# Optimization experiments

Hardware: AMD Instinct MI355X
Metric: run time of the kernel (lower is better)

Reference implementation:

```python
import jax, jax.numpy as jnp
import numpy as np

D_MODEL = 1024
N_HEAD = 16
HEAD_DIM = D_MODEL // N_HEAD


def setup_inputs() -> dict:
    key = jax.random.key(0)
    ks = jax.random.split(key, 11)
    B, L = 1, 2048
    s = 1.0 / np.sqrt(D_MODEL)
    return {
        "q": jax.random.normal(ks[0], (B, L, D_MODEL), jnp.float32),
        "k": jax.random.normal(ks[1], (B, L, D_MODEL), jnp.float32),
        "v": jax.random.normal(ks[2], (B, L, D_MODEL), jnp.float32),
        "w_q": jax.random.normal(ks[3], (D_MODEL, D_MODEL), jnp.float32) * s,
        "b_q": jax.random.normal(ks[4], (D_MODEL,), jnp.float32) * s,
        "w_k": jax.random.normal(ks[5], (D_MODEL, D_MODEL), jnp.float32) * s,
        "b_k": jax.random.normal(ks[6], (D_MODEL,), jnp.float32) * s,
        "w_v": jax.random.normal(ks[7], (D_MODEL, D_MODEL), jnp.float32) * s,
        "b_v": jax.random.normal(ks[8], (D_MODEL,), jnp.float32) * s,
        "w_o": jax.random.normal(ks[9], (D_MODEL, D_MODEL), jnp.float32) * s,
        "b_o": jax.random.normal(ks[10], (D_MODEL,), jnp.float32) * s,
    }


def _split_heads(x):
    # [B, L, D] -> [B, H, L, Dh]
    B, L, D = x.shape
    return x.reshape(B, L, N_HEAD, HEAD_DIM).transpose(0, 2, 1, 3)


def reference(q, k, v, w_q, b_q, w_k, b_k, w_v, b_v, w_o, b_o):
    # Linear projections (torch Linear: x @ W.T + b; here weights stored as [D_in, D_out])
    qh = _split_heads(q @ w_q + b_q)
    kh = _split_heads(k @ w_k + b_k)
    vh = _split_heads(v @ w_v + b_v)
    scale = 1.0 / jnp.sqrt(jnp.asarray(HEAD_DIM, qh.dtype))
    # [B, H, Lq, Lk] full score matrix (faithful to naive implementation)
    score = jnp.einsum("bhqd,bhkd->bhqk", qh, kh) * scale
    attn = jax.nn.softmax(score, axis=-1)
    out = jnp.einsum("bhqk,bhkd->bhqd", attn, vh)
    # concat heads: [B, H, L, Dh] -> [B, L, D]
    B, H, L, Dh = out.shape
    out = out.transpose(0, 2, 1, 3).reshape(B, L, H * Dh)
    return out @ w_o + b_o  # dropout p=0.0 -> identity
```

## Files before the change

### kernel.cpp

```cpp
#include <hip/hip_runtime.h>
#include <hip/hip_bf16.h>
#include <stdint.h>
#include <stddef.h>

typedef __bf16 bf16_t;
typedef __bf16 v8bf __attribute__((ext_vector_type(8)));
typedef __bf16 v4bf __attribute__((ext_vector_type(4)));
typedef float  v4f  __attribute__((ext_vector_type(4)));

#define L_SEQ 2048
#define DM    1024
#define NH    16
#define LOG2E 1.44269504088896340736f
#define SCL   (0.125f * LOG2E)

__device__ __forceinline__ void async_cp16(const void* g, void* l) {
  __builtin_amdgcn_global_load_lds(
      (__attribute__((address_space(1))) void*)(g),
      (__attribute__((address_space(3))) void*)(l),
      16, 0, 0);
}

__device__ __forceinline__ v4f mfma16(v8bf a, v8bf b, v4f c) {
  return __builtin_amdgcn_mfma_f32_16x16x32_bf16(a, b, c, 0, 0, 0);
}

__global__ void k_prep(
    const float* __restrict__ q, const float* __restrict__ k,
    const float* __restrict__ v,
    const float* __restrict__ w0, const float* __restrict__ w1,
    const float* __restrict__ w2, const float* __restrict__ w3,
    bf16_t* __restrict__ Qb, bf16_t* __restrict__ Kb, bf16_t* __restrict__ Vb,
    bf16_t* __restrict__ o0, bf16_t* __restrict__ o1,
    bf16_t* __restrict__ o2, bf16_t* __restrict__ o3)
{
  const int z = blockIdx.z;
  const int tid = threadIdx.x;
  if (z < 4) {
    const float* in = (z == 0) ? w0 : (z == 1) ? w1 : (z == 2) ? w2 : w3;
    bf16_t*     out = (z == 0) ? o0 : (z == 1) ? o1 : (z == 2) ? o2 : o3;
    __shared__ float t[64 * 65];
    const int r0 = blockIdx.y * 64, c0 = blockIdx.x * 64;
#pragma unroll
    for (int p = 0; p < 16; ++p) {
      const int idx = p * 256 + tid;
      const int r = idx >> 6, c = idx & 63;
      t[r * 65 + c] = in[(size_t)(r0 + r) * DM + c0 + c];
    }
    __syncthreads();
#pragma unroll
    for (int p = 0; p < 16; ++p) {
      const int idx = p * 256 + tid;
      const int c = idx >> 6, r = idx & 63;
      out[(size_t)(c0 + c) * DM + r0 + r] = (bf16_t)t[r * 65 + c];
    }
  } else {
    const float* src = (z == 4) ? q : (z == 5) ? k : v;
    bf16_t*      dst = (z == 4) ? Qb : (z == 5) ? Kb : Vb;
    const int n4 = (L_SEQ * DM) / 4;
    const int base = (blockIdx.y * 16 + blockIdx.x) * 256 + tid;
#pragma unroll
    for (int i = base; i < n4; i += 16 * 16 * 256) {
      v4f x = ((const v4f*)src)[i];
      v4bf y;
      y[0] = (bf16_t)x[0]; y[1] = (bf16_t)x[1];
      y[2] = (bf16_t)x[2]; y[3] = (bf16_t)x[3];
      ((v4bf*)dst)[i] = y;
    }
  }
}

__global__ void k_transpose(const bf16_t* __restrict__ in, bf16_t* __restrict__ out,
                            int R, int Cc)
{
  __shared__ bf16_t t[64 * 66];
  const int tid = threadIdx.x;
  const int r0 = blockIdx.y * 64, c0 = blockIdx.x * 64;
#pragma unroll
  for (int p = 0; p < 16; ++p) {
    const int idx = p * 256 + tid;
    const int r = idx >> 6, c = idx & 63;
    t[r * 66 + c] = in[(size_t)(r0 + r) * Cc + c0 + c];
  }
  __syncthreads();
#pragma unroll
  for (int p = 0; p < 16; ++p) {
    const int idx = p * 256 + tid;
    const int c = idx >> 6, r = idx & 63;
    out[(size_t)(c0 + c) * R + r0 + r] = t[r * 66 + c];
  }
}

template <typename OutT>
__device__ __forceinline__ void gemm_body(
    const bf16_t* __restrict__ A, const bf16_t* __restrict__ Bt,
    const float* __restrict__ bias, OutT* __restrict__ C,
    int M, int N, int K, int bx, int by)
{
  __shared__ __align__(16) bf16_t As[2][128 * 64];
  __shared__ __align__(16) bf16_t Bs[2][64 * 64];
  const int tid  = threadIdx.x;
  const int w    = tid >> 6;
  const int lane = tid & 63;
  const int l16  = lane & 15;
  const int q4   = lane >> 4;
  const int m0   = by * 128, n0 = bx * 64;
  const int wm   = (w >> 1) * 64, wn = (w & 1) * 32;

  v4f acc[4][2];
#pragma unroll
  for (int i = 0; i < 4; ++i)
#pragma unroll
    for (int j = 0; j < 2; ++j) {
      v4f z = {0.f, 0.f, 0.f, 0.f};
      acc[i][j] = z;
    }

  const int lr = lane >> 3;
  const int lc = lane & 7;

  auto stage = [&](int k0, int buf) {
#pragma unroll
    for (int c = 0; c < 4; ++c) {
      const int row = 32 * w + 8 * c + lr;
      const int q   = lc ^ (row & 7);
      async_cp16(A + (size_t)(m0 + row) * K + k0 + q * 8,
                 &As[buf][(32 * w + 8 * c) * 64]);
    }
#pragma unroll
    for (int c = 0; c < 2; ++c) {
      const int row = 16 * w + 8 * c + lr;
      const int q   = lc ^ (row & 7);
      async_cp16(Bt + (size_t)(n0 + row) * K + k0 + q * 8,
                 &Bs[buf][(16 * w + 8 * c) * 64]);
    }
  };

  stage(0, 0);
  __syncthreads();

  const int nk = K >> 6;
  for (int kt = 0; kt < nk; ++kt) {
    if (kt + 1 < nk) stage((kt + 1) << 6, (kt + 1) & 1);
    const int buf = kt & 1;
#pragma unroll
    for (int ks = 0; ks < 2; ++ks) {
      v8bf af[4], bf_[2];
#pragma unroll
      for (int mi = 0; mi < 4; ++mi) {
        const int row = wm + mi * 16 + l16;
        const int pc  = (4 * ks + q4) ^ (row & 7);
        af[mi] = *(const v8bf*)(&As[buf][row * 64 + pc * 8]);
      }
#pragma unroll
      for (int ni = 0; ni < 2; ++ni) {
        const int row = wn + ni * 16 + l16;
        const int pc  = (4 * ks + q4) ^ (row & 7);
        bf_[ni] = *(const v8bf*)(&Bs[buf][row * 64 + pc * 8]);
      }
#pragma unroll
      for (int mi = 0; mi < 4; ++mi)
#pragma unroll
        for (int ni = 0; ni < 2; ++ni)
          acc[mi][ni] = mfma16(af[mi], bf_[ni], acc[mi][ni]);
    }
    __syncthreads();
  }

  float bv[2];
#pragma unroll
  for (int ni = 0; ni < 2; ++ni) bv[ni] = bias[n0 + wn + ni * 16 + l16];
#pragma unroll
  for (int mi = 0; mi < 4; ++mi) {
#pragma unroll
    for (int r = 0; r < 4; ++r) {
      const int row = m0 + wm + mi * 16 + q4 * 4 + r;
#pragma unroll
      for (int ni = 0; ni < 2; ++ni) {
        const int col = n0 + wn + ni * 16 + l16;
        C[(size_t)row * N + col] = (OutT)(acc[mi][ni][r] + bv[ni]);
      }
    }
  }
}

__global__ __launch_bounds__(256, 3) void k_gemm_f32out(
    const bf16_t* __restrict__ A, const bf16_t* __restrict__ Bt,
    const float* __restrict__ bias, float* __restrict__ C,
    int M, int N, int K)
{
  gemm_body<float>(A, Bt, bias, C, M, N, K, blockIdx.x, blockIdx.y);
}

__global__ __launch_bounds__(256, 3) void k_gemm_qkv(
    const bf16_t* __restrict__ q, const bf16_t* __restrict__ k,
    const bf16_t* __restrict__ v,
    const bf16_t* __restrict__ wqt, const bf16_t* __restrict__ wkt,
    const bf16_t* __restrict__ wvt,
    const float* __restrict__ bq, const float* __restrict__ bk,
    const float* __restrict__ bv,
    bf16_t* __restrict__ Qp, bf16_t* __restrict__ Kp, bf16_t* __restrict__ Vp)
{
  const int z = blockIdx.z;
  const bf16_t* A    = (z == 0) ? q   : (z == 1) ? k   : v;
  const bf16_t* Bt   = (z == 0) ? wqt : (z == 1) ? wkt : wvt;
  const float*  bias = (z == 0) ? bq  : (z == 1) ? bk  : bv;
  bf16_t*       C    = (z == 0) ? Qp  : (z == 1) ? Kp  : Vp;
  gemm_body<bf16_t>(A, Bt, bias, C, L_SEQ, DM, DM, blockIdx.x, blockIdx.y);
}

__global__ __launch_bounds__(256, 2) void k_attn(
    const bf16_t* __restrict__ Qp,
    const bf16_t* __restrict__ Kp,
    const bf16_t* __restrict__ Vt,
    bf16_t* __restrict__ AO)
{
  const int h  = blockIdx.y;
  const int q0 = blockIdx.x * 64;
  const int tid = threadIdx.x, w = tid >> 6, lane = tid & 63;
  const int l16 = lane & 15, q4 = lane >> 4;
  const int lr = lane >> 3, lc = lane & 7;

  __shared__ __align__(16) bf16_t Qs[64 * 64];
  __shared__ __align__(16) bf16_t Ks[2][64 * 64];
  __shared__ __align__(16) bf16_t Vs[2][64 * 64];
  __shared__ __align__(16) bf16_t Ps[64 * 72];

  auto stage_kv = [&](int j0, int buf) {
#pragma unroll
    for (int c = 0; c < 2; ++c) {
      const int row = 16 * w + 8 * c + lr;
      const int q   = lc ^ (row & 7);
      async_cp16(Kp + (size_t)(j0 + row) * DM + h * 64 + q * 8,
                 &Ks[buf][(16 * w + 8 * c) * 64]);
      async_cp16(Vt + (size_t)(h * 64 + row) * L_SEQ + j0 + q * 8,
                 &Vs[buf][(16 * w + 8 * c) * 64]);
    }
  };

#pragma unroll
  for (int c = 0; c < 2; ++c) {
    const int row = 16 * w + 8 * c + lr;
    const int q   = lc ^ (row & 7);
    async_cp16(Qp + (size_t)(q0 + row) * DM + h * 64 + q * 8,
               &Qs[(16 * w + 8 * c) * 64]);
  }
  stage_kv(0, 0);
  __syncthreads();

  v8bf bq[2];
  {
    const int rowq = 16 * w + l16;
#pragma unroll
    for (int ks = 0; ks < 2; ++ks) {
      const int pc = (4 * ks + q4) ^ (rowq & 7);
      bq[ks] = *(const v8bf*)(&Qs[rowq * 64 + pc * 8]);
    }
  }

  float m_run = -1e30f, l_run = 0.f;
  v4f od[4];
#pragma unroll
  for (int d = 0; d < 4; ++d) { v4f z = {0.f,0.f,0.f,0.f}; od[d] = z; }

  const int prow = 16 * w + l16;

  for (int jt = 0; jt < L_SEQ / 64; ++jt) {
    if (jt + 1 < L_SEQ / 64) stage_kv((jt + 1) * 64, (jt + 1) & 1);
    const int buf = jt & 1;

    v4f st[4];
#pragma unroll
    for (int nf = 0; nf < 4; ++nf) {
      v4f a0 = {0.f, 0.f, 0.f, 0.f};
#pragma unroll
      for (int ks = 0; ks < 2; ++ks) {
        const int rowk = nf * 16 + l16;
        const int pc   = (4 * ks + q4) ^ (rowk & 7);
        v8bf ak = *(const v8bf*)(&Ks[buf][rowk * 64 + pc * 8]);
        a0 = mfma16(ak, bq[ks], a0);
      }
      st[nf] = a0;
    }

    float mx = st[0][0];
#pragma unroll
    for (int nf = 0; nf < 4; ++nf)
#pragma unroll
      for (int r = 0; r < 4; ++r) mx = fmaxf(mx, st[nf][r]);
    mx = fmaxf(mx, __shfl_xor(mx, 16, 64));
    mx = fmaxf(mx, __shfl_xor(mx, 32, 64));
    const float mn    = fmaxf(m_run, mx);
    const float alpha = exp2f((m_run - mn) * SCL);
    const float mnS   = mn * SCL;
    m_run = mn;

    float ps = 0.f;
#pragma unroll
    for (int nf = 0; nf < 4; ++nf) {
      v4bf pb;
#pragma unroll
      for (int r = 0; r < 4; ++r) {
        const float p = exp2f(fmaf(st[nf][r], SCL, -mnS));
        ps += p;
        pb[r] = (bf16_t)p;
      }
      *(v4bf*)(&Ps[prow * 72 + nf * 16 + q4 * 4]) = pb;
    }
    l_run = l_run * alpha + ps;
#pragma unroll
    for (int d = 0; d < 4; ++d)
#pragma unroll
      for (int r = 0; r < 4; ++r) od[d][r] *= alpha;

#pragma unroll
    for (int ks = 0; ks < 2; ++ks) {
      v8bf bp = *(const v8bf*)(&Ps[prow * 72 + ks * 32 + q4 * 8]);
#pragma unroll
      for (int dd = 0; dd < 4; ++dd) {
        const int rowv = dd * 16 + l16;
        const int pc   = (4 * ks + q4) ^ (rowv & 7);
        v8bf av = *(const v8bf*)(&Vs[buf][rowv * 64 + pc * 8]);
        od[dd] = mfma16(av, bp, od[dd]);
      }
    }
    __syncthreads();
  }

  l_run += __shfl_xor(l_run, 16, 64);
  l_run += __shfl_xor(l_run, 32, 64);
  const float inv = 1.f / l_run;

  const int rowo = q0 + 16 * w + l16;
#pragma unroll
  for (int dd = 0; dd < 4; ++dd) {
    v4bf ob;
#pragma unroll
    for (int r = 0; r < 4; ++r) ob[r] = (bf16_t)(od[dd][r] * inv);
    *(v4bf*)(&AO[(size_t)rowo * DM + h * 64 + dd * 16 + q4 * 4]) = ob;
  }
}

extern "C" void kernel_launch(void* const* d_in, const int* in_sizes, int n_in,
                              void* d_out, int out_size, void* d_ws, size_t ws_size,
                              hipStream_t stream)
{
  const float* q  = (const float*)d_in[0];
  const float* k  = (const float*)d_in[1];
  const float* v  = (const float*)d_in[2];
  const float* wq = (const float*)d_in[3];
  const float* bq = (const float*)d_in[4];
  const float* wk = (const float*)d_in[5];
  const float* bk = (const float*)d_in[6];
  const float* wv = (const float*)d_in[7];
  const float* bv = (const float*)d_in[8];
  const float* wo = (const float*)d_in[9];
  const float* bo = (const float*)d_in[10];
  float* out = (float*)d_out;

  bf16_t* ws  = (bf16_t*)d_ws;
  bf16_t* Qb  = ws;
  bf16_t* Kb  = Qb  + (size_t)L_SEQ * DM;
  bf16_t* Vb  = Kb  + (size_t)L_SEQ * DM;
  bf16_t* Qp  = Vb  + (size_t)L_SEQ * DM;
  bf16_t* Kp  = Qp  + (size_t)L_SEQ * DM;
  bf16_t* Vp  = Kp  + (size_t)L_SEQ * DM;
  bf16_t* Vtr = Vp  + (size_t)L_SEQ * DM;
  bf16_t* AO  = Vtr + (size_t)L_SEQ * DM;
  bf16_t* Wqt = AO  + (size_t)L_SEQ * DM;
  bf16_t* Wkt = Wqt + (size_t)DM * DM;
  bf16_t* Wvt = Wkt + (size_t)DM * DM;
  bf16_t* Wot = Wvt + (size_t)DM * DM;

  k_prep<<<dim3(16, 16, 7), 256, 0, stream>>>(q, k, v, wq, wk, wv, wo,
                                              Qb, Kb, Vb, Wqt, Wkt, Wvt, Wot);
  k_gemm_qkv<<<dim3(16, 16, 3), 256, 0, stream>>>(Qb, Kb, Vb, Wqt, Wkt, Wvt,
                                                  bq, bk, bv, Qp, Kp, Vp);
  k_transpose<<<dim3(16, 32), 256, 0, stream>>>(Vp, Vtr, L_SEQ, DM);
  k_attn<<<dim3(32, 16), 256, 0, stream>>>(Qp, Kp, Vtr, AO);
  k_gemm_f32out<<<dim3(16, 16), 256, 0, stream>>>(AO, Wot, bo, out,
                                                  L_SEQ, DM, DM);
}
```

Measured before the change: 188.0 us.

## Retile GEMMs to 128-wide N with K=32 stages and halve attention block warps

The GEMM body becomes templated on the per-warp M extent. It uses 128-column N tiles and 32-deep K stages with a new swizzle and precomputed global pointers, so each warp holds a larger accumulator tile and reuses fragments more. The QKV GEMM uses 128x128 tiles and the output GEMM 64x128, with the grids adjusted to match. The attention kernel now runs 2 warps per block, each handling 32 query rows as two 16-row groups, so every K/V fragment read from LDS feeds two MFMAs. In exchange there is more register pressure, fewer blocks in flight, and twice as many K-loop barriers in the GEMMs.

```diff
diff --git a/kernel.cpp b/kernel.cpp
--- a/kernel.cpp
+++ b/kernel.cpp
@@ -91,92 +91,98 @@
   }
 }
 
-template <typename OutT>
+template <int MW, typename OutT>
 __device__ __forceinline__ void gemm_body(
     const bf16_t* __restrict__ A, const bf16_t* __restrict__ Bt,
     const float* __restrict__ bias, OutT* __restrict__ C,
     int M, int N, int K, int bx, int by)
 {
-  __shared__ __align__(16) bf16_t As[2][128 * 64];
-  __shared__ __align__(16) bf16_t Bs[2][64 * 64];
+  constexpr int MT = 2 * MW;
+  constexpr int CA = MW / 32;
+  constexpr int MI = MW / 16;
+  __shared__ __align__(16) bf16_t As[2][MT * 32];
+  __shared__ __align__(16) bf16_t Bs[2][128 * 32];
   const int tid  = threadIdx.x;
   const int w    = tid >> 6;
   const int lane = tid & 63;
   const int l16  = lane & 15;
   const int q4   = lane >> 4;
-  const int m0   = by * 128, n0 = bx * 64;
-  const int wm   = (w >> 1) * 64, wn = (w & 1) * 32;
-
-  v4f acc[4][2];
-#pragma unroll
-  for (int i = 0; i < 4; ++i)
-#pragma unroll
-    for (int j = 0; j < 2; ++j) {
+  const int m0   = by * MT, n0 = bx * 128;
+  const int wm   = (w >> 1) * MW, wn = (w & 1) * 64;
+
+  v4f acc[MI][4];
+#pragma unroll
+  for (int i = 0; i < MI; ++i)
+#pragma unroll
+    for (int j = 0; j < 4; ++j) {
       v4f z = {0.f, 0.f, 0.f, 0.f};
       acc[i][j] = z;
     }
 
-  const int lr = lane >> 3;
-  const int lc = lane & 7;
+  const int srow = lane >> 2;
+  const int sq   = lane & 3;
+  const bf16_t* pA[CA];
+  const bf16_t* pB[2];
+#pragma unroll
+  for (int c = 0; c < CA; ++c) {
+    const int row = (MW / 2) * w + 16 * c + srow;
+    const int q   = sq ^ ((row >> 1) & 3);
+    pA[c] = A + (size_t)(m0 + row) * K + q * 8;
+  }
+#pragma unroll
+  for (int c = 0; c < 2; ++c) {
+    const int row = 32 * w + 16 * c + srow;
+    const int q   = sq ^ ((row >> 1) & 3);
+    pB[c] = Bt + (size_t)(n0 + row) * K + q * 8;
+  }
 
   auto stage = [&](int k0, int buf) {
 #pragma unroll
-    for (int c = 0; c < 4; ++c) {
-      const int row = 32 * w + 8 * c + lr;
-      const int q   = lc ^ (row & 7);
-      async_cp16(A + (size_t)(m0 + row) * K + k0 + q * 8,
-                 &As[buf][(32 * w + 8 * c) * 64]);
-    }
-#pragma unroll
-    for (int c = 0; c < 2; ++c) {
-      const int row = 16 * w + 8 * c + lr;
-      const int q   = lc ^ (row & 7);
-      async_cp16(Bt + (size_t)(n0 + row) * K + k0 + q * 8,
-                 &Bs[buf][(16 * w + 8 * c) * 64]);
-    }
+    for (int c = 0; c < CA; ++c)
+      async_cp16(pA[c] + k0, &As[buf][((MW / 2) * w + 16 * c) * 32]);
+#pragma unroll
+    for (int c = 0; c < 2; ++c)
+      async_cp16(pB[c] + k0, &Bs[buf][(32 * w + 16 * c) * 32]);
   };
 
   stage(0, 0);
   __syncthreads();
 
-  const int nk = K >> 6;
+  const int nk = K >> 5;
   for (int kt = 0; kt < nk; ++kt) {
-    if (kt + 1 < nk) stage((kt + 1) << 6, (kt + 1) & 1);
+    if (kt + 1 < nk) stage((kt + 1) << 5, (kt + 1) & 1);
     const int buf = kt & 1;
-#pragma unroll
-    for (int ks = 0; ks < 2; ++ks) {
-      v8bf af[4], bf_[2];
-#pragma unroll
-      for (int mi = 0; mi < 4; ++mi) {
-        const int row = wm + mi * 16 + l16;
-        const int pc  = (4 * ks + q4) ^ (row & 7);
-        af[mi] = *(const v8bf*)(&As[buf][row * 64 + pc * 8]);
-      }
-#pragma unroll
-      for (int ni = 0; ni < 2; ++ni) {
-        const int row = wn + ni * 16 + l16;
-        const int pc  = (4 * ks + q4) ^ (row & 7);
-        bf_[ni] = *(const v8bf*)(&Bs[buf][row * 64 + pc * 8]);
-      }
-#pragma unroll
-      for (int mi = 0; mi < 4; ++mi)
-#pragma unroll
-        for (int ni = 0; ni < 2; ++ni)
-          acc[mi][ni] = mfma16(af[mi], bf_[ni], acc[mi][ni]);
-    }
+    v8bf af[MI], bfr[4];
+#pragma unroll
+    for (int mi = 0; mi < MI; ++mi) {
+      const int row = wm + mi * 16 + l16;
+      const int qq  = q4 ^ ((row >> 1) & 3);
+      af[mi] = *(const v8bf*)(&As[buf][row * 32 + qq * 8]);
+    }
+#pragma unroll
+    for (int ni = 0; ni < 4; ++ni) {
+      const int row = wn + ni * 16 + l16;
+      const int qq  = q4 ^ ((row >> 1) & 3);
+      bfr[ni] = *(const v8bf*)(&Bs[buf][row * 32 + qq * 8]);
+    }
+#pragma unroll
+    for (int mi = 0; mi < MI; ++mi)
+#pragma unroll
+      for (int ni = 0; ni < 4; ++ni)
+        acc[mi][ni] = mfma16(af[mi], bfr[ni], acc[mi][ni]);
     __syncthreads();
   }
 
-  float bv[2];
-#pragma unroll
-  for (int ni = 0; ni < 2; ++ni) bv[ni] = bias[n0 + wn + ni * 16 + l16];
-#pragma unroll
-  for (int mi = 0; mi < 4; ++mi) {
+  float bv[4];
+#pragma unroll
+  for (int ni = 0; ni < 4; ++ni) bv[ni] = bias[n0 + wn + ni * 16 + l16];
+#pragma unroll
+  for (int mi = 0; mi < MI; ++mi) {
 #pragma unroll
     for (int r = 0; r < 4; ++r) {
       const int row = m0 + wm + mi * 16 + q4 * 4 + r;
 #pragma unroll
-      for (int ni = 0; ni < 2; ++ni) {
+      for (int ni = 0; ni < 4; ++ni) {
         const int col = n0 + wn + ni * 16 + l16;
         C[(size_t)row * N + col] = (OutT)(acc[mi][ni][r] + bv[ni]);
       }
@@ -184,15 +190,15 @@
   }
 }
 
-__global__ __launch_bounds__(256, 3) void k_gemm_f32out(
+__global__ __launch_bounds__(256, 2) void k_gemm_f32out(
     const bf16_t* __restrict__ A, const bf16_t* __restrict__ Bt,
     const float* __restrict__ bias, float* __restrict__ C,
     int M, int N, int K)
 {
-  gemm_body<float>(A, Bt, bias, C, M, N, K, blockIdx.x, blockIdx.y);
-}
-
-__global__ __launch_bounds__(256, 3) void k_gemm_qkv(
+  gemm_body<32, float>(A, Bt, bias, C, M, N, K, blockIdx.x, blockIdx.y);
+}
+
+__global__ __launch_bounds__(256, 2) void k_gemm_qkv(
     const bf16_t* __restrict__ q, const bf16_t* __restrict__ k,
     const bf16_t* __restrict__ v,
     const bf16_t* __restrict__ wqt, const bf16_t* __restrict__ wkt,
@@ -206,10 +212,10 @@
   const bf16_t* Bt   = (z == 0) ? wqt : (z == 1) ? wkt : wvt;
   const float*  bias = (z == 0) ? bq  : (z == 1) ? bk  : bv;
   bf16_t*       C    = (z == 0) ? Qp  : (z == 1) ? Kp  : Vp;
-  gemm_body<bf16_t>(A, Bt, bias, C, L_SEQ, DM, DM, blockIdx.x, blockIdx.y);
-}
-
-__global__ __launch_bounds__(256, 2) void k_attn(
+  gemm_body<64, bf16_t>(A, Bt, bias, C, L_SEQ, DM, DM, blockIdx.x, blockIdx.y);
+}
+
+__global__ __launch_bounds__(128, 2) void k_attn(
     const bf16_t* __restrict__ Qp,
     const bf16_t* __restrict__ Kp,
     const bf16_t* __restrict__ Vt,
@@ -226,118 +232,138 @@
   __shared__ __align__(16) bf16_t Vs[2][64 * 64];
   __shared__ __align__(16) bf16_t Ps[64 * 72];
 
+  const bf16_t* pK[4];
+  const bf16_t* pV[4];
+#pragma unroll
+  for (int c = 0; c < 4; ++c) {
+    const int row = 32 * w + 8 * c + lr;
+    const int q   = lc ^ (row & 7);
+    pK[c] = Kp + (size_t)row * DM + h * 64 + q * 8;
+    pV[c] = Vt + (size_t)(h * 64 + row) * L_SEQ + q * 8;
+  }
   auto stage_kv = [&](int j0, int buf) {
 #pragma unroll
-    for (int c = 0; c < 2; ++c) {
-      const int row = 16 * w + 8 * c + lr;
-      const int q   = lc ^ (row & 7);
-      async_cp16(Kp + (size_t)(j0 + row) * DM + h * 64 + q * 8,
-                 &Ks[buf][(16 * w + 8 * c) * 64]);
-      async_cp16(Vt + (size_t)(h * 64 + row) * L_SEQ + j0 + q * 8,
-                 &Vs[buf][(16 * w + 8 * c) * 64]);
+    for (int c = 0; c < 4; ++c) {
+      async_cp16(pK[c] + (size_t)j0 * DM, &Ks[buf][(32 * w + 8 * c) * 64]);
+      async_cp16(pV[c] + j0,              &Vs[buf][(32 * w + 8 * c) * 64]);
     }
   };
 
 #pragma unroll
-  for (int c = 0; c < 2; ++c) {
-    const int row = 16 * w + 8 * c + lr;
+  for (int c = 0; c < 4; ++c) {
+    const int row = 32 * w + 8 * c + lr;
     const int q   = lc ^ (row & 7);
     async_cp16(Qp + (size_t)(q0 + row) * DM + h * 64 + q * 8,
-               &Qs[(16 * w + 8 * c) * 64]);
+               &Qs[(32 * w + 8 * c) * 64]);
   }
   stage_kv(0, 0);
   __syncthreads();
 
-  v8bf bq[2];
-  {
-    const int rowq = 16 * w + l16;
+  v8bf bq[2][2];
+  const int prow0 = 32 * w + l16;
+  const int prow1 = 32 * w + 16 + l16;
+#pragma unroll
+  for (int g = 0; g < 2; ++g) {
+    const int rowq = 32 * w + 16 * g + l16;
 #pragma unroll
     for (int ks = 0; ks < 2; ++ks) {
       const int pc = (4 * ks + q4) ^ (rowq & 7);
-      bq[ks] = *(const v8bf*)(&Qs[rowq * 64 + pc * 8]);
-    }
-  }
-
-  float m_run = -1e30f, l_run = 0.f;
-  v4f od[4];
-#pragma unroll
-  for (int d = 0; d < 4; ++d) { v4f z = {0.f,0.f,0.f,0.f}; od[d] = z; }
-
-  const int prow = 16 * w + l16;
+      bq[g][ks] = *(const v8bf*)(&Qs[rowq * 64 + pc * 8]);
+    }
+  }
+
+  float m_run[2] = {-1e30f, -1e30f}, l_run[2] = {0.f, 0.f};
+  v4f od[2][4];
+#pragma unroll
+  for (int g = 0; g < 2; ++g)
+#pragma unroll
+    for (int d = 0; d < 4; ++d) { v4f z = {0.f,0.f,0.f,0.f}; od[g][d] = z; }
 
   for (int jt = 0; jt < L_SEQ / 64; ++jt) {
     if (jt + 1 < L_SEQ / 64) stage_kv((jt + 1) * 64, (jt + 1) & 1);
     const int buf = jt & 1;
 
-    v4f st[4];
+    v4f st[2][4];
+#pragma unroll
+    for (int g = 0; g < 2; ++g)
+#pragma unroll
+      for (int nf = 0; nf < 4; ++nf) { v4f z = {0.f,0.f,0.f,0.f}; st[g][nf] = z; }
 #pragma unroll
     for (int nf = 0; nf < 4; ++nf) {
-      v4f a0 = {0.f, 0.f, 0.f, 0.f};
+      const int rowk = nf * 16 + l16;
 #pragma unroll
       for (int ks = 0; ks < 2; ++ks) {
-        const int rowk = nf * 16 + l16;
-        const int pc   = (4 * ks + q4) ^ (rowk & 7);
+        const int pc = (4 * ks + q4) ^ (rowk & 7);
         v8bf ak = *(const v8bf*)(&Ks[buf][rowk * 64 + pc * 8]);
-        a0 = mfma16(ak, bq[ks], a0);
+        st[0][nf] = mfma16(ak, bq[0][ks], st[0][nf]);
+        st[1][nf] = mfma16(ak, bq[1][ks], st[1][nf]);
       }
-      st[nf] = a0;
-    }
-
-    float mx = st[0][0];
-#pragma unroll
-    for (int nf = 0; nf < 4; ++nf)
-#pragma unroll
-      for (int r = 0; r < 4; ++r) mx = fmaxf(mx, st[nf][r]);
-    mx = fmaxf(mx, __shfl_xor(mx, 16, 64));
-    mx = fmaxf(mx, __shfl_xor(mx, 32, 64));
-    const float mn    = fmaxf(m_run, mx);
-    const float alpha = exp2f((m_run - mn) * SCL);
-    const float mnS   = mn * SCL;
-    m_run = mn;
-
-    float ps = 0.f;
-#pragma unroll
-    for (int nf = 0; nf < 4; ++nf) {
-      v4bf pb;
-#pragma unroll
-      for (int r = 0; r < 4; ++r) {
-        const float p = exp2f(fmaf(st[nf][r], SCL, -mnS));
-        ps += p;
-        pb[r] = (bf16_t)p;
+    }
+
+#pragma unroll
+    for (int g = 0; g < 2; ++g) {
+      float mx = st[g][0][0];
+#pragma unroll
+      for (int nf = 0; nf < 4; ++nf)
+#pragma unroll
+        for (int r = 0; r < 4; ++r) mx = fmaxf(mx, st[g][nf][r]);
+      mx = fmaxf(mx, __shfl_xor(mx, 16, 64));
+      mx = fmaxf(mx, __shfl_xor(mx, 32, 64));
+      const float mn    = fmaxf(m_run[g], mx);
+      const float alpha = exp2f((m_run[g] - mn) * SCL);
+      const float mnS   = mn * SCL;
+      m_run[g] = mn;
+
+      const int prow = (g == 0) ? prow0 : prow1;
+      float ps = 0.f;
+#pragma unroll
+      for (int nf = 0; nf < 4; ++nf) {
+        v4bf pb;
+#pragma unroll
+        for (int r = 0; r < 4; ++r) {
+          const float p = exp2f(fmaf(st[g][nf][r], SCL, -mnS));
+          ps += p;
+          pb[r] = (bf16_t)p;
+        }
+        *(v4bf*)(&Ps[prow * 72 + nf * 16 + q4 * 4]) = pb;
       }
-      *(v4bf*)(&Ps[prow * 72 + nf * 16 + q4 * 4]) = pb;
-    }
-    l_run = l_run * alpha + ps;
-#pragma unroll
-    for (int d = 0; d < 4; ++d)
-#pragma unroll
-      for (int r = 0; r < 4; ++r) od[d][r] *= alpha;
+      l_run[g] = l_run[g] * alpha + ps;
+#pragma unroll
+      for (int d = 0; d < 4; ++d)
+#pragma unroll
+        for (int r = 0; r < 4; ++r) od[g][d][r] *= alpha;
+    }
 
 #pragma unroll
     for (int ks = 0; ks < 2; ++ks) {
-      v8bf bp = *(const v8bf*)(&Ps[prow * 72 + ks * 32 + q4 * 8]);
+      v8bf bp0 = *(const v8bf*)(&Ps[prow0 * 72 + ks * 32 + q4 * 8]);
+      v8bf bp1 = *(const v8bf*)(&Ps[prow1 * 72 + ks * 32 + q4 * 8]);
 #pragma unroll
       for (int dd = 0; dd < 4; ++dd) {
         const int rowv = dd * 16 + l16;
         const int pc   = (4 * ks + q4) ^ (rowv & 7);
         v8bf av = *(const v8bf*)(&Vs[buf][rowv * 64 + pc * 8]);
-        od[dd] = mfma16(av, bp, od[dd]);
+        od[0][dd] = mfma16(av, bp0, od[0][dd]);
+        od[1][dd] = mfma16(av, bp1, od[1][dd]);
       }
     }
     __syncthreads();
   }
 
-  l_run += __shfl_xor(l_run, 16, 64);
-  l_run += __shfl_xor(l_run, 32, 64);
-  const float inv = 1.f / l_run;
-
-  const int rowo = q0 + 16 * w + l16;
-#pragma unroll
-  for (int dd = 0; dd < 4; ++dd) {
-    v4bf ob;
-#pragma unroll
-    for (int r = 0; r < 4; ++r) ob[r] = (bf16_t)(od[dd][r] * inv);
-    *(v4bf*)(&AO[(size_t)rowo * DM + h * 64 + dd * 16 + q4 * 4]) = ob;
+#pragma unroll
+  for (int g = 0; g < 2; ++g) {
+    float l = l_run[g];
+    l += __shfl_xor(l, 16, 64);
+    l += __shfl_xor(l, 32, 64);
+    const float inv = 1.f / l;
+    const int rowo = q0 + 32 * w + 16 * g + l16;
+#pragma unroll
+    for (int dd = 0; dd < 4; ++dd) {
+      v4bf ob;
+#pragma unroll
+      for (int r = 0; r < 4; ++r) ob[r] = (bf16_t)(od[g][dd][r] * inv);
+      *(v4bf*)(&AO[(size_t)rowo * DM + h * 64 + dd * 16 + q4 * 4]) = ob;
+    }
   }
 }
 
@@ -374,10 +400,10 @@
 
   k_prep<<<dim3(16, 16, 7), 256, 0, stream>>>(q, k, v, wq, wk, wv, wo,
                                               Qb, Kb, Vb, Wqt, Wkt, Wvt, Wot);
-  k_gemm_qkv<<<dim3(16, 16, 3), 256, 0, stream>>>(Qb, Kb, Vb, Wqt, Wkt, Wvt,
-                                                  bq, bk, bv, Qp, Kp, Vp);
+  k_gemm_qkv<<<dim3(8, 16, 3), 256, 0, stream>>>(Qb, Kb, Vb, Wqt, Wkt, Wvt,
+                                                 bq, bk, bv, Qp, Kp, Vp);
   k_transpose<<<dim3(16, 32), 256, 0, stream>>>(Vp, Vtr, L_SEQ, DM);
-  k_attn<<<dim3(32, 16), 256, 0, stream>>>(Qp, Kp, Vtr, AO);
-  k_gemm_f32out<<<dim3(16, 16), 256, 0, stream>>>(AO, Wot, bo, out,
-                                                  L_SEQ, DM, DM);
-}
+  k_attn<<<dim3(32, 16), 128, 0, stream>>>(Qp, Kp, Vtr, AO);
+  k_gemm_f32out<<<dim3(8, 32), 256, 0, stream>>>(AO, Wot, bo, out,
+                                                 L_SEQ, DM, DM);
+}
```

Measured after the change: 223.8 us. 1.19x slower.

## Fuse V transpose into projection GEMM, shrink attention blocks, use fast exp2

Applied to the files above, without the earlier changes.

Computes V's projection directly in transposed form (W_v^T times V^T with a per-row bias), which removes the separate transpose kernel. Q and K projections now write into one interleaved buffer with row stride 2*DM, and all projection tiles launch as a single 1D grid of 768 blocks. The attention kernel moves to 128-thread blocks with 32 query rows each and an interleaved head order, doubling the grid to 1024 blocks, and the Q and P shared buffers are merged. It also switches to the hardware exp2 builtin. The Wqt/Wkt adjacency assumption and the bk - DM pointer trick depend on the workspace layout.

```diff
diff --git a/kernel.cpp b/kernel.cpp
--- a/kernel.cpp
+++ b/kernel.cpp
@@ -24,6 +24,12 @@
 __device__ __forceinline__ v4f mfma16(v8bf a, v8bf b, v4f c) {
   return __builtin_amdgcn_mfma_f32_16x16x32_bf16(a, b, c, 0, 0, 0);
 }
+
+#if __has_builtin(__builtin_amdgcn_exp2f)
+__device__ __forceinline__ float fast_exp2(float x) { return __builtin_amdgcn_exp2f(x); }
+#else
+__device__ __forceinline__ float fast_exp2(float x) { return exp2f(x); }
+#endif
 
 __global__ void k_prep(
     const float* __restrict__ q, const float* __restrict__ k,
@@ -70,32 +76,11 @@
   }
 }
 
-__global__ void k_transpose(const bf16_t* __restrict__ in, bf16_t* __restrict__ out,
-                            int R, int Cc)
-{
-  __shared__ bf16_t t[64 * 66];
-  const int tid = threadIdx.x;
-  const int r0 = blockIdx.y * 64, c0 = blockIdx.x * 64;
-#pragma unroll
-  for (int p = 0; p < 16; ++p) {
-    const int idx = p * 256 + tid;
-    const int r = idx >> 6, c = idx & 63;
-    t[r * 66 + c] = in[(size_t)(r0 + r) * Cc + c0 + c];
-  }
-  __syncthreads();
-#pragma unroll
-  for (int p = 0; p < 16; ++p) {
-    const int idx = p * 256 + tid;
-    const int c = idx >> 6, r = idx & 63;
-    out[(size_t)(c0 + c) * R + r0 + r] = t[r * 66 + c];
-  }
-}
-
 template <typename OutT>
-__device__ __forceinline__ void gemm_body(
+__device__ __forceinline__ void gemm128x64_body(
     const bf16_t* __restrict__ A, const bf16_t* __restrict__ Bt,
-    const float* __restrict__ bias, OutT* __restrict__ C,
-    int M, int N, int K, int bx, int by)
+    const float* __restrict__ biasN, const float* __restrict__ biasM,
+    OutT* __restrict__ C, int M, int N, int K, int bx, int by)
 {
   __shared__ __align__(16) bf16_t As[2][128 * 64];
   __shared__ __align__(16) bf16_t Bs[2][64 * 64];
@@ -106,6 +91,7 @@
   const int q4   = lane >> 4;
   const int m0   = by * 128, n0 = bx * 64;
   const int wm   = (w >> 1) * 64, wn = (w & 1) * 32;
+  const int lr = lane >> 3, lc = lane & 7;
 
   v4f acc[4][2];
 #pragma unroll
@@ -115,9 +101,6 @@
       v4f z = {0.f, 0.f, 0.f, 0.f};
       acc[i][j] = z;
     }
-
-  const int lr = lane >> 3;
-  const int lc = lane & 7;
 
   auto stage = [&](int k0, int buf) {
 #pragma unroll
@@ -167,74 +150,97 @@
     __syncthreads();
   }
 
-  float bv[2];
-#pragma unroll
-  for (int ni = 0; ni < 2; ++ni) bv[ni] = bias[n0 + wn + ni * 16 + l16];
+  float bvn[2] = {0.f, 0.f};
+  if (biasN) {
+#pragma unroll
+    for (int ni = 0; ni < 2; ++ni) bvn[ni] = biasN[n0 + wn + ni * 16 + l16];
+  }
 #pragma unroll
   for (int mi = 0; mi < 4; ++mi) {
 #pragma unroll
     for (int r = 0; r < 4; ++r) {
       const int row = m0 + wm + mi * 16 + q4 * 4 + r;
+      const float bm = biasM ? biasM[row] : 0.f;
 #pragma unroll
       for (int ni = 0; ni < 2; ++ni) {
         const int col = n0 + wn + ni * 16 + l16;
-        C[(size_t)row * N + col] = (OutT)(acc[mi][ni][r] + bv[ni]);
-      }
-    }
-  }
-}
-
-__global__ __launch_bounds__(256, 3) void k_gemm_f32out(
-    const bf16_t* __restrict__ A, const bf16_t* __restrict__ Bt,
-    const float* __restrict__ bias, float* __restrict__ C,
-    int M, int N, int K)
-{
-  gemm_body<float>(A, Bt, bias, C, M, N, K, blockIdx.x, blockIdx.y);
-}
-
-__global__ __launch_bounds__(256, 3) void k_gemm_qkv(
-    const bf16_t* __restrict__ q, const bf16_t* __restrict__ k,
-    const bf16_t* __restrict__ v,
-    const bf16_t* __restrict__ wqt, const bf16_t* __restrict__ wkt,
-    const bf16_t* __restrict__ wvt,
+        C[(size_t)row * N + col] = (OutT)(acc[mi][ni][r] + bvn[ni] + bm);
+      }
+    }
+  }
+}
+
+__global__ __launch_bounds__(256, 3) void k_gemm_fused(
+    const bf16_t* __restrict__ Qb, const bf16_t* __restrict__ Kb,
+    const bf16_t* __restrict__ Vb,
+    const bf16_t* __restrict__ Wqkt,
+    const bf16_t* __restrict__ Wvt,
     const float* __restrict__ bq, const float* __restrict__ bk,
     const float* __restrict__ bv,
-    bf16_t* __restrict__ Qp, bf16_t* __restrict__ Kp, bf16_t* __restrict__ Vp)
-{
-  const int z = blockIdx.z;
-  const bf16_t* A    = (z == 0) ? q   : (z == 1) ? k   : v;
-  const bf16_t* Bt   = (z == 0) ? wqt : (z == 1) ? wkt : wvt;
-  const float*  bias = (z == 0) ? bq  : (z == 1) ? bk  : bv;
-  bf16_t*       C    = (z == 0) ? Qp  : (z == 1) ? Kp  : Vp;
-  gemm_body<bf16_t>(A, Bt, bias, C, L_SEQ, DM, DM, blockIdx.x, blockIdx.y);
-}
-
-__global__ __launch_bounds__(256, 2) void k_attn(
-    const bf16_t* __restrict__ Qp,
-    const bf16_t* __restrict__ Kp,
+    bf16_t* __restrict__ QKo, bf16_t* __restrict__ Vtr)
+{
+  const int idx = blockIdx.x;
+  const bf16_t *A, *Bt;
+  const float *bN = nullptr, *bM = nullptr;
+  bf16_t* C;
+  int M, N, bx, by;
+  if (idx < 512) {
+    by = idx & 15; bx = idx >> 4;
+    A  = (bx < 16) ? Qb : Kb;
+    Bt = Wqkt;
+    bN = (bx < 16) ? bq : (bk - DM);
+    C  = QKo; M = L_SEQ; N = 2 * DM;
+  } else {
+    const int i2 = idx - 512;
+    by = i2 & 7; bx = i2 >> 3;
+    A  = Wvt; Bt = Vb; bM = bv;
+    C  = Vtr; M = DM; N = L_SEQ;
+  }
+  gemm128x64_body<bf16_t>(A, Bt, bN, bM, C, M, N, DM, bx, by);
+}
+
+__global__ __launch_bounds__(256, 3) void k_gemm_oproj(
+    const bf16_t* __restrict__ A, const bf16_t* __restrict__ Bt,
+    const float* __restrict__ bias, float* __restrict__ C)
+{
+  gemm128x64_body<float>(A, Bt, bias, nullptr, C, L_SEQ, DM, DM,
+                         blockIdx.x, blockIdx.y);
+}
+
+__global__ __launch_bounds__(128, 2) void k_attn(
+    const bf16_t* __restrict__ QKp,
     const bf16_t* __restrict__ Vt,
     bf16_t* __restrict__ AO)
 {
-  const int h  = blockIdx.y;
-  const int q0 = blockIdx.x * 64;
+  constexpr int LD = 2 * DM;
+  const int lid = blockIdx.x;
+  const int h   = (lid & 7) + 8 * ((lid >> 3) & 1);
+  const int q0  = (lid >> 4) * 32;
   const int tid = threadIdx.x, w = tid >> 6, lane = tid & 63;
   const int l16 = lane & 15, q4 = lane >> 4;
   const int lr = lane >> 3, lc = lane & 7;
 
-  __shared__ __align__(16) bf16_t Qs[64 * 64];
   __shared__ __align__(16) bf16_t Ks[2][64 * 64];
   __shared__ __align__(16) bf16_t Vs[2][64 * 64];
-  __shared__ __align__(16) bf16_t Ps[64 * 72];
-
+  __shared__ __align__(16) bf16_t QPs[32 * 72];
+
+  const bf16_t* Qp = QKp;
+  const bf16_t* Kp = QKp + DM;
+
+  const bf16_t* pK[4];
+  const bf16_t* pV[4];
+#pragma unroll
+  for (int c = 0; c < 4; ++c) {
+    const int row = 32 * w + 8 * c + lr;
+    const int q   = lc ^ (row & 7);
+    pK[c] = Kp + (size_t)row * LD + h * 64 + q * 8;
+    pV[c] = Vt + (size_t)(h * 64 + row) * L_SEQ + q * 8;
+  }
   auto stage_kv = [&](int j0, int buf) {
 #pragma unroll
-    for (int c = 0; c < 2; ++c) {
-      const int row = 16 * w + 8 * c + lr;
-      const int q   = lc ^ (row & 7);
-      async_cp16(Kp + (size_t)(j0 + row) * DM + h * 64 + q * 8,
-                 &Ks[buf][(16 * w + 8 * c) * 64]);
-      async_cp16(Vt + (size_t)(h * 64 + row) * L_SEQ + j0 + q * 8,
-                 &Vs[buf][(16 * w + 8 * c) * 64]);
+    for (int c = 0; c < 4; ++c) {
+      async_cp16(pK[c] + (size_t)j0 * LD, &Ks[buf][(32 * w + 8 * c) * 64]);
+      async_cp16(pV[c] + j0,              &Vs[buf][(32 * w + 8 * c) * 64]);
     }
   };
 
@@ -242,28 +248,25 @@
   for (int c = 0; c < 2; ++c) {
     const int row = 16 * w + 8 * c + lr;
     const int q   = lc ^ (row & 7);
-    async_cp16(Qp + (size_t)(q0 + row) * DM + h * 64 + q * 8,
-               &Qs[(16 * w + 8 * c) * 64]);
+    async_cp16(Qp + (size_t)(q0 + row) * LD + h * 64 + q * 8,
+               &QPs[(16 * w + 8 * c) * 64]);
   }
   stage_kv(0, 0);
   __syncthreads();
 
+  const int prow = 16 * w + l16;
   v8bf bq[2];
-  {
-    const int rowq = 16 * w + l16;
-#pragma unroll
-    for (int ks = 0; ks < 2; ++ks) {
-      const int pc = (4 * ks + q4) ^ (rowq & 7);
-      bq[ks] = *(const v8bf*)(&Qs[rowq * 64 + pc * 8]);
-    }
-  }
+#pragma unroll
+  for (int ks = 0; ks < 2; ++ks) {
+    const int pc = (4 * ks + q4) ^ (prow & 7);
+    bq[ks] = *(const v8bf*)(&QPs[prow * 64 + pc * 8]);
+  }
+  __syncthreads();
 
   float m_run = -1e30f, l_run = 0.f;
   v4f od[4];
 #pragma unroll
-  for (int d = 0; d < 4; ++d) { v4f z = {0.f,0.f,0.f,0.f}; od[d] = z; }
-
-  const int prow = 16 * w + l16;
+  for (int d = 0; d < 4; ++d) { v4f z = {0.f, 0.f, 0.f, 0.f}; od[d] = z; }
 
   for (int jt = 0; jt < L_SEQ / 64; ++jt) {
     if (jt + 1 < L_SEQ / 64) stage_kv((jt + 1) * 64, (jt + 1) & 1);
@@ -273,10 +276,10 @@
 #pragma unroll
     for (int nf = 0; nf < 4; ++nf) {
       v4f a0 = {0.f, 0.f, 0.f, 0.f};
+      const int rowk = nf * 16 + l16;
 #pragma unroll
       for (int ks = 0; ks < 2; ++ks) {
-        const int rowk = nf * 16 + l16;
-        const int pc   = (4 * ks + q4) ^ (rowk & 7);
+        const int pc = (4 * ks + q4) ^ (rowk & 7);
         v8bf ak = *(const v8bf*)(&Ks[buf][rowk * 64 + pc * 8]);
         a0 = mfma16(ak, bq[ks], a0);
       }
@@ -291,7 +294,7 @@
     mx = fmaxf(mx, __shfl_xor(mx, 16, 64));
     mx = fmaxf(mx, __shfl_xor(mx, 32, 64));
     const float mn    = fmaxf(m_run, mx);
-    const float alpha = exp2f((m_run - mn) * SCL);
+    const float alpha = fast_exp2((m_run - mn) * SCL);
     const float mnS   = mn * SCL;
     m_run = mn;
 
@@ -301,11 +304,11 @@
       v4bf pb;
 #pragma unroll
       for (int r = 0; r < 4; ++r) {
-        const float p = exp2f(fmaf(st[nf][r], SCL, -mnS));
+        const float p = fast_exp2(fmaf(st[nf][r], SCL, -mnS));
         ps += p;
         pb[r] = (bf16_t)p;
       }
-      *(v4bf*)(&Ps[prow * 72 + nf * 16 + q4 * 4]) = pb;
+      *(v4bf*)(&QPs[prow * 72 + nf * 16 + q4 * 4]) = pb;
     }
     l_run = l_run * alpha + ps;
 #pragma unroll
@@ -315,7 +318,7 @@
 
 #pragma unroll
     for (int ks = 0; ks < 2; ++ks) {
-      v8bf bp = *(const v8bf*)(&Ps[prow * 72 + ks * 32 + q4 * 8]);
+      v8bf bp = *(const v8bf*)(&QPs[prow * 72 + ks * 32 + q4 * 8]);
 #pragma unroll
       for (int dd = 0; dd < 4; ++dd) {
         const int rowv = dd * 16 + l16;
@@ -330,8 +333,7 @@
   l_run += __shfl_xor(l_run, 16, 64);
   l_run += __shfl_xor(l_run, 32, 64);
   const float inv = 1.f / l_run;
-
-  const int rowo = q0 + 16 * w + l16;
+  const int rowo = q0 + prow;
 #pragma unroll
   for (int dd = 0; dd < 4; ++dd) {
     v4bf ob;
@@ -358,26 +360,23 @@
   const float* bo = (const float*)d_in[10];
   float* out = (float*)d_out;
 
-  bf16_t* ws  = (bf16_t*)d_ws;
-  bf16_t* Qb  = ws;
-  bf16_t* Kb  = Qb  + (size_t)L_SEQ * DM;
-  bf16_t* Vb  = Kb  + (size_t)L_SEQ * DM;
-  bf16_t* Qp  = Vb  + (size_t)L_SEQ * DM;
-  bf16_t* Kp  = Qp  + (size_t)L_SEQ * DM;
-  bf16_t* Vp  = Kp  + (size_t)L_SEQ * DM;
-  bf16_t* Vtr = Vp  + (size_t)L_SEQ * DM;
-  bf16_t* AO  = Vtr + (size_t)L_SEQ * DM;
-  bf16_t* Wqt = AO  + (size_t)L_SEQ * DM;
-  bf16_t* Wkt = Wqt + (size_t)DM * DM;
-  bf16_t* Wvt = Wkt + (size_t)DM * DM;
-  bf16_t* Wot = Wvt + (size_t)DM * DM;
+  const size_t SZ = (size_t)L_SEQ * DM;
+  bf16_t* ws   = (bf16_t*)d_ws;
+  bf16_t* Qb   = ws;
+  bf16_t* Kb   = Qb + SZ;
+  bf16_t* Vb   = Kb + SZ;
+  bf16_t* QK   = Vb + SZ;
+  bf16_t* Vtr  = QK + 2 * SZ;
+  bf16_t* AO   = Vtr + SZ;
+  bf16_t* Wqt  = AO + SZ;
+  bf16_t* Wkt  = Wqt + (size_t)DM * DM;
+  bf16_t* Wvt  = Wkt + (size_t)DM * DM;
+  bf16_t* Wot  = Wvt + (size_t)DM * DM;
 
   k_prep<<<dim3(16, 16, 7), 256, 0, stream>>>(q, k, v, wq, wk, wv, wo,
                                               Qb, Kb, Vb, Wqt, Wkt, Wvt, Wot);
-  k_gemm_qkv<<<dim3(16, 16, 3), 256, 0, stream>>>(Qb, Kb, Vb, Wqt, Wkt, Wvt,
-                                                  bq, bk, bv, Qp, Kp, Vp);
-  k_transpose<<<dim3(16, 32), 256, 0, stream>>>(Vp, Vtr, L_SEQ, DM);
-  k_attn<<<dim3(32, 16), 256, 0, stream>>>(Qp, Kp, Vtr, AO);
-  k_gemm_f32out<<<dim3(16, 16), 256, 0, stream>>>(AO, Wot, bo, out,
-                                                  L_SEQ, DM, DM);
-}
+  k_gemm_fused<<<dim3(768), 256, 0, stream>>>(Qb, Kb, Vb, Wqt, Wvt,
+                                              bq, bk, bv, QK, Vtr);
+  k_attn<<<dim3(1024), 128, 0, stream>>>(QK, Vtr, AO);
+  k_gemm_oproj<<<dim3(16, 16), 256, 0, stream>>>(AO, Wot, bo, out);
+}
```

Measured after the change: 182.0 us. 1.03x faster.
